# Kernel optimization log

Hardware: AMD Instinct MI355X
Metric: run time of the kernel (lower is better)

The kernel has to match this reference:

```python
import jax, jax.numpy as jnp
import numpy as np

B, S, HID = 1, 2048, 2048
H, KV, D = 16, 8, 128          # heads, kv heads, head_dim
EPS = 1e-6
THETA_T, THETA_HW = 1000000.0, 10000.0
SCALE = D ** -0.5
NEG = -1e9


def _rms(x, w):
    xf = x.astype(jnp.float32)
    var = jnp.mean(xf * xf, axis=-1, keepdims=True)
    return (w * (xf * jax.lax.rsqrt(var + EPS))).astype(x.dtype)


def _rope_cs(pos, theta, half_dim):
    # Module builds RoPE with head_dim = 2*half_dim then takes every-other freq:
    # exponents arange(0, 2*half_dim, 4) / (2*half_dim)  -> half_dim//2 freqs
    dim2 = 2 * half_dim
    inv_freq = 1.0 / theta ** (jnp.arange(0, dim2, 4, dtype=jnp.float32) / dim2)
    freqs = pos.astype(jnp.float32)[:, None] * inv_freq[None, :]   # [S, half_dim//2]
    emb = jnp.concatenate([freqs, freqs], axis=-1)                 # [S, half_dim]
    return jnp.cos(emb), jnp.sin(emb)


def _rot_half(x):
    d = x.shape[-1] // 2
    return jnp.concatenate([-x[..., d:], x[..., :d]], axis=-1)


def _apply_rope(q, k, cos, sin):
    cos = cos[None, None]  # [1,1,S,dim]
    sin = sin[None, None]
    return q * cos + _rot_half(q) * sin, k * cos + _rot_half(k) * sin


def setup_inputs() -> dict:
    key = jax.random.key(0)
    ks = jax.random.split(key, 10)
    hidden_states = jax.random.normal(ks[0], (B, S, HID), jnp.float32)
    indexes = jax.random.randint(ks[1], (3, S), 0, S)
    causal = jnp.tril(jnp.ones((S, S), bool))
    attention_mask = jnp.where(causal, 0.0, NEG).astype(jnp.float32)[None, None]
    qkv_w = jax.random.normal(ks[2], ((H + 2 * KV) * D, HID), jnp.float32) * 0.02
    qkv_b = jax.random.normal(ks[3], ((H + 2 * KV) * D,), jnp.float32) * 0.02
    o_w = jax.random.normal(ks[4], (HID, H * D), jnp.float32) * 0.02
    o_b = jax.random.normal(ks[5], (HID,), jnp.float32) * 0.02
    q_norm_w = jnp.ones((D // 2,), jnp.float32)
    k_norm_w = jnp.ones((D // 2,), jnp.float32)
    q_norm_hw_w = jnp.ones((D // 2,), jnp.float32)
    k_norm_hw_w = jnp.ones((D // 2,), jnp.float32)
    return dict(hidden_states=hidden_states, indexes=indexes, attention_mask=attention_mask,
                qkv_w=qkv_w, qkv_b=qkv_b, o_w=o_w, o_b=o_b,
                q_norm_w=q_norm_w, k_norm_w=k_norm_w,
                q_norm_hw_w=q_norm_hw_w, k_norm_hw_w=k_norm_hw_w)


def reference(hidden_states, indexes, attention_mask, qkv_w, qkv_b, o_w, o_b,
              q_norm_w, k_norm_w, q_norm_hw_w, k_norm_hw_w):
    b, s, _ = hidden_states.shape
    qkv = hidden_states @ qkv_w.T + qkv_b
    q, k, v = jnp.split(qkv, [H * D, H * D + KV * D], axis=-1)
    q = q.reshape(b, s, H, D)
    k = k.reshape(b, s, KV, D)
    v = v.reshape(b, s, KV, D)

    # split head_dim into time half and hw half
    q_t, q_hw = jnp.split(q, 2, axis=-1)
    k_t, k_hw = jnp.split(k, 2, axis=-1)
    q_t = jnp.swapaxes(_rms(q_t, q_norm_w), 1, 2)       # [B,H,S,D/2]
    k_t = jnp.swapaxes(_rms(k_t, k_norm_w), 1, 2)
    q_hw = jnp.swapaxes(_rms(q_hw, q_norm_hw_w), 1, 2)
    k_hw = jnp.swapaxes(_rms(k_hw, k_norm_hw_w), 1, 2)
    q_h, q_ww = jnp.split(q_hw, 2, axis=-1)             # [B,H,S,D/4]
    k_h, k_ww = jnp.split(k_hw, 2, axis=-1)

    cos_t, sin_t = _rope_cs(indexes[0], THETA_T, D // 2)
    q_t, k_t = _apply_rope(q_t, k_t, cos_t, sin_t)
    cos_h, sin_h = _rope_cs(indexes[1], THETA_HW, D // 4)
    q_h, k_h = _apply_rope(q_h, k_h, cos_h, sin_h)
    cos_w, sin_w = _rope_cs(indexes[2], THETA_HW, D // 4)
    q_ww, k_ww = _apply_rope(q_ww, k_ww, cos_w, sin_w)

    query = jnp.concatenate([q_t, q_h, q_ww], axis=-1)  # [B,H,S,D]
    keyst = jnp.concatenate([k_t, k_h, k_ww], axis=-1)  # [B,KV,S,D]
    value = jnp.swapaxes(v, 1, 2)                       # [B,KV,S,D]

    n_rep = H // KV
    keyst = jnp.repeat(keyst, n_rep, axis=1)
    value = jnp.repeat(value, n_rep, axis=1)

    scores = jnp.einsum('bhsd,bhtd->bhst', query, keyst) * SCALE + attention_mask
    probs = jax.nn.softmax(scores.astype(jnp.float32), axis=-1).astype(query.dtype)
    attn = jnp.einsum('bhst,bhtd->bhsd', probs, value)
    attn = jnp.swapaxes(attn, 1, 2).reshape(b, s, H * D)
    return attn @ o_w.T + o_b
```

## Files before the change

### kernel.cpp

```cpp
#include <hip/hip_runtime.h>

typedef __bf16 bf16;
typedef __bf16 bf16x4 __attribute__((ext_vector_type(4)));
typedef __bf16 bf16x8 __attribute__((ext_vector_type(8)));
typedef float f32x4 __attribute__((ext_vector_type(4)));

#define S_LEN 2048
#define HIDDEN 2048
#define NH 16
#define NKV 8
#define HD 128
#define QKV_N 4096

__device__ __forceinline__ void async_load16(const void* g, void* l) {
  __builtin_amdgcn_global_load_lds((const __attribute__((address_space(1))) unsigned int*)g,
                                   (__attribute__((address_space(3))) unsigned int*)l,
                                   16, 0, 0);
}

template <int C>
__device__ __forceinline__ float dpp_f(float x) {
  return __builtin_bit_cast(float, __builtin_amdgcn_mov_dpp(
      __builtin_bit_cast(int, x), C, 0xF, 0xF, true));
}
__device__ __forceinline__ float rowmax16(float x) {
  x = fmaxf(x, dpp_f<0x128>(x));
  x = fmaxf(x, dpp_f<0x124>(x));
  x = fmaxf(x, dpp_f<0x122>(x));
  x = fmaxf(x, dpp_f<0x121>(x));
  return x;
}
__device__ __forceinline__ float rowsum16(float x) {
  x += dpp_f<0x128>(x);
  x += dpp_f<0x124>(x);
  x += dpp_f<0x122>(x);
  x += dpp_f<0x121>(x);
  return x;
}

__global__ __launch_bounds__(256)
void cvt_f32_bf16(const float* __restrict__ src, bf16* __restrict__ dst, int n) {
  int i = (blockIdx.x * 256 + threadIdx.x) * 4;
  if (i < n) {
    float4 v = *(const float4*)(src + i);
    bf16x4 o = {(bf16)v.x, (bf16)v.y, (bf16)v.z, (bf16)v.w};
    *(bf16x4*)(dst + i) = o;
  }
}

template <int WRITE_BF16>
__global__ __launch_bounds__(256)
void gemm_bt(const bf16* __restrict__ A, const bf16* __restrict__ B,
             const float* __restrict__ bias, void* __restrict__ Cout,
             int M, int N, int K) {
  __shared__ bf16 As[128 * 32];
  __shared__ bf16 Bs[128 * 32];
  const int tid = threadIdx.x;
  const int w = tid >> 6, lane = tid & 63;
  const int quad = lane >> 4, l15 = lane & 15;
  const int wm = w >> 1, wn = w & 1;
  const int m0 = blockIdx.y * 128, n0 = blockIdx.x * 128;

  f32x4 acc[4][4];
#pragma unroll
  for (int i = 0; i < 4; i++)
#pragma unroll
    for (int j = 0; j < 4; j++) acc[i][j] = (f32x4){0.f, 0.f, 0.f, 0.f};

  const int crow = lane >> 2;
  const int ccol = (lane & 3) * 8;

  for (int k0 = 0; k0 < K; k0 += 32) {
    __syncthreads();
#pragma unroll
    for (int q = 0; q < 2; q++) {
      int c = 2 * w + q;
      async_load16(A + (size_t)(m0 + c * 16 + crow) * K + k0 + ccol, (char*)As + c * 1024);
      async_load16(B + (size_t)(n0 + c * 16 + crow) * K + k0 + ccol, (char*)Bs + c * 1024);
    }
    __syncthreads();
    bf16x8 af[4], bfr[4];
#pragma unroll
    for (int i = 0; i < 4; i++)
      af[i] = *(const bf16x8*)(As + (wm * 64 + i * 16 + l15) * 32 + quad * 8);
#pragma unroll
    for (int j = 0; j < 4; j++)
      bfr[j] = *(const bf16x8*)(Bs + (wn * 64 + j * 16 + l15) * 32 + quad * 8);
#pragma unroll
    for (int i = 0; i < 4; i++)
#pragma unroll
      for (int j = 0; j < 4; j++)
        acc[i][j] = __builtin_amdgcn_mfma_f32_16x16x32_bf16(af[i], bfr[j], acc[i][j], 0, 0, 0);
  }

#pragma unroll
  for (int i = 0; i < 4; i++) {
#pragma unroll
    for (int j = 0; j < 4; j++) {
      int col = n0 + wn * 64 + j * 16 + l15;
      float bv = bias[col];
#pragma unroll
      for (int r = 0; r < 4; r++) {
        int row = m0 + wm * 64 + i * 16 + quad * 4 + r;
        float v = acc[i][j][r] + bv;
        if (WRITE_BF16)
          ((bf16*)Cout)[(size_t)row * N + col] = (bf16)v;
        else
          ((float*)Cout)[(size_t)row * N + col] = v;
      }
    }
  }
}

__global__ __launch_bounds__(256)
void gemm_bt64(const bf16* __restrict__ A, const bf16* __restrict__ B,
               const float* __restrict__ bias, float* __restrict__ Cout,
               int M, int N, int K) {
  __shared__ bf16 As[128 * 32];
  __shared__ bf16 Bs[64 * 32];
  const int tid = threadIdx.x;
  const int w = tid >> 6, lane = tid & 63;
  const int quad = lane >> 4, l15 = lane & 15;
  const int m0 = blockIdx.y * 128, n0 = blockIdx.x * 64;

  f32x4 acc[2][4];
#pragma unroll
  for (int i = 0; i < 2; i++)
#pragma unroll
    for (int j = 0; j < 4; j++) acc[i][j] = (f32x4){0.f, 0.f, 0.f, 0.f};

  const int crow = lane >> 2;
  const int ccol = (lane & 3) * 8;

  for (int k0 = 0; k0 < K; k0 += 32) {
    __syncthreads();
#pragma unroll
    for (int q = 0; q < 2; q++) {
      int c = 2 * w + q;
      async_load16(A + (size_t)(m0 + c * 16 + crow) * K + k0 + ccol, (char*)As + c * 1024);
    }
    async_load16(B + (size_t)(n0 + w * 16 + crow) * K + k0 + ccol, (char*)Bs + w * 1024);
    __syncthreads();
    bf16x8 af[2], bfr[4];
#pragma unroll
    for (int i = 0; i < 2; i++)
      af[i] = *(const bf16x8*)(As + (w * 32 + i * 16 + l15) * 32 + quad * 8);
#pragma unroll
    for (int j = 0; j < 4; j++)
      bfr[j] = *(const bf16x8*)(Bs + (j * 16 + l15) * 32 + quad * 8);
#pragma unroll
    for (int i = 0; i < 2; i++)
#pragma unroll
      for (int j = 0; j < 4; j++)
        acc[i][j] = __builtin_amdgcn_mfma_f32_16x16x32_bf16(af[i], bfr[j], acc[i][j], 0, 0, 0);
  }

#pragma unroll
  for (int i = 0; i < 2; i++) {
#pragma unroll
    for (int j = 0; j < 4; j++) {
      int col = n0 + j * 16 + l15;
      float bv = bias[col];
#pragma unroll
      for (int r = 0; r < 4; r++) {
        int row = m0 + w * 32 + i * 16 + quad * 4 + r;
        Cout[(size_t)row * N + col] = acc[i][j][r] + bv;
      }
    }
  }
}

__global__ __launch_bounds__(128)
void normrope(const bf16* __restrict__ qkv, const int* __restrict__ idx,
              const float* __restrict__ qnw, const float* __restrict__ knw,
              const float* __restrict__ qnhw, const float* __restrict__ knhw,
              bf16* __restrict__ Qb, bf16* __restrict__ Kb) {
  const int s = blockIdx.x;
  const int y = blockIdx.y;
  const int d = threadIdx.x;

  const bool isq = (y < 16);
  const int off = isq ? (y * HD + d) : (2048 + (y - 16) * HD + d);
  float x = (float)qkv[(size_t)s * QKV_N + off];

  float ss = x * x;
#pragma unroll
  for (int o = 32; o; o >>= 1) ss += __shfl_xor(ss, o);
  float inv = rsqrtf(ss * (1.f / 64.f) + 1e-6f);
  const float* wt = (d < 64) ? (isq ? qnw : knw) : (isq ? qnhw : knhw);
  float yn = x * inv * wt[d & 63];

  float pos, invf;
  int xorm;
  bool firsthalf;
  if (d < 64) {
    pos = (float)idx[s];
    int i = d & 31;
    invf = exp2f(-(float)i * 0.6228615177913804f);
    xorm = 32;
    firsthalf = (d < 32);
  } else {
    int j = d - 64;
    int region = j >> 5;
    pos = (float)idx[(1 + region) * S_LEN + s];
    int i = j & 15;
    invf = exp2f(-(float)i * 0.8304820237218406f);
    xorm = 16;
    firsthalf = ((j & 31) < 16);
  }
  float ang = pos * invf;
  float si, co;
  sincosf(ang, &si, &co);
  float partner = __shfl_xor(yn, xorm);
  float outv = firsthalf ? (yn * co - partner * si) : (yn * co + partner * si);

  if (isq)
    Qb[((size_t)y * S_LEN + s) * HD + d] = (bf16)outv;
  else
    Kb[((size_t)(y - 16) * S_LEN + s) * HD + d] = (bf16)outv;
}

__global__ __launch_bounds__(256)
void vtrans(const bf16* __restrict__ qkv, bf16* __restrict__ VT) {
  __shared__ bf16 T[64][72];
  const int tid = threadIdx.x;
  const int s0 = blockIdx.x * 64, d0 = blockIdx.y * 64, kv = blockIdx.z;
#pragma unroll
  for (int it = 0; it < 2; it++) {
    int r = (tid >> 3) + it * 32;
    int c = (tid & 7) * 8;
    bf16x8 v = *(const bf16x8*)(qkv + (size_t)(s0 + r) * QKV_N + 3072 + kv * HD + d0 + c);
    *(bf16x8*)(&T[r][c]) = v;
  }
  __syncthreads();
#pragma unroll
  for (int it = 0; it < 2; it++) {
    int r = (tid >> 3) + it * 32;
    int c = (tid & 7) * 8;
    bf16x8 o;
#pragma unroll
    for (int j = 0; j < 8; j++) o[j] = T[c + j][r];
    *(bf16x8*)(VT + ((size_t)kv * HD + d0 + r) * S_LEN + s0 + c) = o;
  }
}

__global__ __launch_bounds__(256)
void attn_fused(const bf16* __restrict__ Qb, const bf16* __restrict__ Kb,
                const bf16* __restrict__ VT, bf16* __restrict__ attnO) {
  __shared__ bf16 Kbuf[2][8192];
  __shared__ bf16 Vbuf[8192];
  __shared__ __align__(16) bf16 Ps[4][16][72];
  const int tid = threadIdx.x;
  const int w = tid >> 6, lane = tid & 63;
  const int quad = lane >> 4, l15 = lane & 15;
  const int b = blockIdx.x;
  const int h = b & 15;
  const int g = b >> 4;
  const int qb64 = (g < 16) ? (31 - g) : (g - 16);
  const int nT = qb64 + 1;
  const int qr0 = qb64 * 64 + w * 16;
  const int kv = h >> 1;

  const bf16* Qg = Qb + (size_t)h * S_LEN * HD;
  const bf16* Kg = Kb + (size_t)kv * S_LEN * HD;
  const bf16* Vg = VT + (size_t)kv * HD * S_LEN;

  const bf16* ksrc = Kg + (size_t)(w * 16 + l15) * HD + quad * 8;
  const bf16* vsrc = Vg + (size_t)(2 * w * 16 + l15) * S_LEN + quad * 8;

  bf16x8 aq[4];
#pragma unroll
  for (int kc = 0; kc < 4; kc++)
    aq[kc] = *(const bf16x8*)(Qg + (size_t)(qr0 + l15) * HD + kc * 32 + quad * 8);

  float m2[4], li[4];
  f32x4 Oacc[8];
#pragma unroll
  for (int r = 0; r < 4; r++) { m2[r] = -1e30f; li[r] = 0.f; }
#pragma unroll
  for (int dt = 0; dt < 8; dt++) Oacc[dt] = (f32x4){0.f, 0.f, 0.f, 0.f};

  const float SC2 = 0.12751745f;

#pragma unroll
  for (int kc = 0; kc < 4; kc++)
    async_load16(ksrc + kc * 32, (char*)Kbuf[0] + (w * 4 + kc) * 1024);

  for (int tt = 0; tt < nT; ++tt) {
    const int t0 = tt << 6;
    const int cur = tt & 1;
    const bool more = (tt + 1 < nT);
    __asm__ __volatile__("s_waitcnt vmcnt(0)" ::: "memory");
    __syncthreads();

#pragma unroll
    for (int e = 0; e < 2; e++)
#pragma unroll
      for (int half = 0; half < 2; half++)
        async_load16(vsrc + (size_t)e * 16 * S_LEN + t0 + half * 32,
                     (char*)Vbuf + (half * 8 + 2 * w + e) * 1024);
    if (more) {
#pragma unroll
      for (int kc = 0; kc < 4; kc++)
        async_load16(ksrc + (size_t)(t0 + 64) * HD + kc * 32,
                     (char*)Kbuf[cur ^ 1] + (w * 4 + kc) * 1024);
    }

    f32x4 sacc[4];
#pragma unroll
    for (int nt = 0; nt < 4; nt++) {
      sacc[nt] = (f32x4){0.f, 0.f, 0.f, 0.f};
#pragma unroll
      for (int kc = 0; kc < 4; kc++) {
        bf16x8 bk = *(const bf16x8*)((const char*)Kbuf[cur] + (nt * 4 + kc) * 1024 + lane * 16);
        sacc[nt] = __builtin_amdgcn_mfma_f32_16x16x32_bf16(aq[kc], bk, sacc[nt], 0, 0, 0);
      }
    }

    const bool full = (t0 + 64 <= qr0);
#pragma unroll
    for (int r = 0; r < 4; r++) {
      const int mrow = qr0 + quad * 4 + r;
      float s0 = sacc[0][r] * SC2, s1 = sacc[1][r] * SC2;
      float s2 = sacc[2][r] * SC2, s3 = sacc[3][r] * SC2;
      if (!full) {
        int cb = t0 + l15;
        if (cb > mrow) s0 = -1e30f;
        if (cb + 16 > mrow) s1 = -1e30f;
        if (cb + 32 > mrow) s2 = -1e30f;
        if (cb + 48 > mrow) s3 = -1e30f;
      }
      float mx = rowmax16(fmaxf(fmaxf(s0, s1), fmaxf(s2, s3)));
      float mnew = fmaxf(m2[r], mx);
      float alpha = exp2f(m2[r] - mnew);
      float p0 = exp2f(s0 - mnew), p1 = exp2f(s1 - mnew);
      float p2 = exp2f(s2 - mnew), p3 = exp2f(s3 - mnew);
      float rs = rowsum16((p0 + p1) + (p2 + p3));
      li[r] = li[r] * alpha + rs;
      m2[r] = mnew;
#pragma unroll
      for (int dt = 0; dt < 8; dt++) Oacc[dt][r] *= alpha;
      Ps[w][quad * 4 + r][l15] = (bf16)p0;
      Ps[w][quad * 4 + r][16 + l15] = (bf16)p1;
      Ps[w][quad * 4 + r][32 + l15] = (bf16)p2;
      Ps[w][quad * 4 + r][48 + l15] = (bf16)p3;
    }
    __asm__ __volatile__("s_waitcnt lgkmcnt(0)" ::: "memory");
    if (more)
      __asm__ __volatile__("s_waitcnt vmcnt(4)" ::: "memory");
    else
      __asm__ __volatile__("s_waitcnt vmcnt(0)" ::: "memory");

#pragma unroll
    for (int half = 0; half < 2; half++) {
      bf16x8 ap = *(const bf16x8*)(&Ps[w][l15][half * 32 + quad * 8]);
#pragma unroll
      for (int dt = 0; dt < 8; dt++) {
        bf16x8 bv = *(const bf16x8*)((const char*)Vbuf + (half * 8 + dt) * 1024 + lane * 16);
        Oacc[dt] = __builtin_amdgcn_mfma_f32_16x16x32_bf16(ap, bv, Oacc[dt], 0, 0, 0);
      }
    }
  }

#pragma unroll
  for (int r = 0; r < 4; r++) {
    float invl = 1.f / li[r];
    int srow = qr0 + quad * 4 + r;
#pragma unroll
    for (int dt = 0; dt < 8; dt++)
      attnO[(size_t)srow * HIDDEN + h * HD + dt * 16 + l15] = (bf16)(Oacc[dt][r] * invl);
  }
}

extern "C" void kernel_launch(void* const* d_in, const int* in_sizes, int n_in,
                              void* d_out, int out_size, void* d_ws, size_t ws_size,
                              hipStream_t stream) {
  const float* hidden = (const float*)d_in[0];
  const int* idx = (const int*)d_in[1];
  const float* qkv_w = (const float*)d_in[3];
  const float* qkv_b = (const float*)d_in[4];
  const float* o_w = (const float*)d_in[5];
  const float* o_b = (const float*)d_in[6];
  const float* qnw = (const float*)d_in[7];
  const float* knw = (const float*)d_in[8];
  const float* qnhw = (const float*)d_in[9];
  const float* knhw = (const float*)d_in[10];

  char* ws = (char*)d_ws;
  bf16* hB   = (bf16*)(ws);
  bf16* qwB  = (bf16*)(ws + (8u << 20));
  bf16* qkvB = (bf16*)(ws + (24u << 20));
  bf16* Qb   = (bf16*)(ws + (40u << 20));
  bf16* Kb   = (bf16*)(ws + (48u << 20));
  bf16* VT   = (bf16*)(ws + (52u << 20));
  bf16* owB  = hB;
  bf16* attn = qwB;

  cvt_f32_bf16<<<HIDDEN * S_LEN / 1024, 256, 0, stream>>>(hidden, hB, HIDDEN * S_LEN);
  cvt_f32_bf16<<<QKV_N * HIDDEN / 1024, 256, 0, stream>>>(qkv_w, qwB, QKV_N * HIDDEN);

  gemm_bt<1><<<dim3(QKV_N / 128, S_LEN / 128), 256, 0, stream>>>(
      hB, qwB, qkv_b, qkvB, S_LEN, QKV_N, HIDDEN);

  cvt_f32_bf16<<<HIDDEN * HIDDEN / 1024, 256, 0, stream>>>(o_w, owB, HIDDEN * HIDDEN);

  normrope<<<dim3(S_LEN, 24), 128, 0, stream>>>(qkvB, idx, qnw, knw, qnhw, knhw, Qb, Kb);
  vtrans<<<dim3(S_LEN / 64, HD / 64, NKV), 256, 0, stream>>>(qkvB, VT);

  attn_fused<<<512, 256, 0, stream>>>(Qb, Kb, VT, attn);

  gemm_bt64<<<dim3(HIDDEN / 64, S_LEN / 128), 256, 0, stream>>>(
      attn, owB, o_b, (float*)d_out, S_LEN, HIDDEN, HIDDEN);
}
```

Measured before the change: 310.6 us.

## Split attention KV range across two wave groups and merge partial softmax

Doubles the attention block to 512 threads. Two groups of four waves each process half of the key tiles for the same query rows, and their partial O, max and sum values are merged through LDS at the end. V is now loaded directly into registers instead of staged in LDS. The softmax scale is folded into Q during the norm/rope step, and rescaling is skipped unless the row max grows by more than a threshold (lazy rescale). This adds parallelism per block and drops the per-element scale multiply, at the cost of losing the cross-tile K prefetch pipeline, adding extra syncs per iteration and higher register pressure.

```diff
diff --git a/kernel.cpp b/kernel.cpp
--- a/kernel.cpp
+++ b/kernel.cpp
@@ -215,7 +215,7 @@
   float outv = firsthalf ? (yn * co - partner * si) : (yn * co + partner * si);
 
   if (isq)
-    Qb[((size_t)y * S_LEN + s) * HD + d] = (bf16)outv;
+    Qb[((size_t)y * S_LEN + s) * HD + d] = (bf16)(outv * 0.12751745f);
   else
     Kb[((size_t)(y - 16) * S_LEN + s) * HD + d] = (bf16)outv;
 }
@@ -244,29 +244,31 @@
   }
 }
 
-__global__ __launch_bounds__(256)
+__global__ __launch_bounds__(512, 4)
 void attn_fused(const bf16* __restrict__ Qb, const bf16* __restrict__ Kb,
                 const bf16* __restrict__ VT, bf16* __restrict__ attnO) {
   __shared__ bf16 Kbuf[2][8192];
-  __shared__ bf16 Vbuf[8192];
-  __shared__ __align__(16) bf16 Ps[4][16][72];
+  __shared__ __align__(16) bf16 Ps[8][16][72];
   const int tid = threadIdx.x;
   const int w = tid >> 6, lane = tid & 63;
   const int quad = lane >> 4, l15 = lane & 15;
+  const int wq = w & 3, grp = w >> 2;
   const int b = blockIdx.x;
   const int h = b & 15;
   const int g = b >> 4;
   const int qb64 = (g < 16) ? (31 - g) : (g - 16);
   const int nT = qb64 + 1;
-  const int qr0 = qb64 * 64 + w * 16;
+  const int nH = nT >> 1;
+  const int L = nT - nH;
+  const int qr0 = qb64 * 64 + wq * 16;
   const int kv = h >> 1;
 
   const bf16* Qg = Qb + (size_t)h * S_LEN * HD;
   const bf16* Kg = Kb + (size_t)kv * S_LEN * HD;
   const bf16* Vg = VT + (size_t)kv * HD * S_LEN;
 
-  const bf16* ksrc = Kg + (size_t)(w * 16 + l15) * HD + quad * 8;
-  const bf16* vsrc = Vg + (size_t)(2 * w * 16 + l15) * S_LEN + quad * 8;
+  const bf16* ksrc = Kg + (size_t)(wq * 16 + l15) * HD + quad * 8;
+  const bf16* vsrc = Vg + (size_t)l15 * S_LEN + quad * 8;
 
   bf16x8 aq[4];
 #pragma unroll
@@ -280,31 +282,25 @@
 #pragma unroll
   for (int dt = 0; dt < 8; dt++) Oacc[dt] = (f32x4){0.f, 0.f, 0.f, 0.f};
 
-  const float SC2 = 0.12751745f;
-
-#pragma unroll
-  for (int kc = 0; kc < 4; kc++)
-    async_load16(ksrc + kc * 32, (char*)Kbuf[0] + (w * 4 + kc) * 1024);
-
-  for (int tt = 0; tt < nT; ++tt) {
-    const int t0 = tt << 6;
-    const int cur = tt & 1;
-    const bool more = (tt + 1 < nT);
+  for (int u = 0; u < L; ++u) {
+    const int tIdx = grp ? (nH + u) : u;
+    const bool active = grp || (u < nH);
+    const int t0 = tIdx << 6;
+
+    __syncthreads();
+    bf16x8 v0[8];
+    if (active) {
+#pragma unroll
+      for (int kc = 0; kc < 4; kc++)
+        async_load16(ksrc + (size_t)t0 * HD + kc * 32,
+                     (char*)Kbuf[grp] + (wq * 4 + kc) * 1024);
+#pragma unroll
+      for (int dt = 0; dt < 8; dt++)
+        v0[dt] = *(const bf16x8*)(vsrc + (size_t)dt * 16 * S_LEN + t0);
+    }
     __asm__ __volatile__("s_waitcnt vmcnt(0)" ::: "memory");
     __syncthreads();
-
-#pragma unroll
-    for (int e = 0; e < 2; e++)
-#pragma unroll
-      for (int half = 0; half < 2; half++)
-        async_load16(vsrc + (size_t)e * 16 * S_LEN + t0 + half * 32,
-                     (char*)Vbuf + (half * 8 + 2 * w + e) * 1024);
-    if (more) {
-#pragma unroll
-      for (int kc = 0; kc < 4; kc++)
-        async_load16(ksrc + (size_t)(t0 + 64) * HD + kc * 32,
-                     (char*)Kbuf[cur ^ 1] + (w * 4 + kc) * 1024);
-    }
+    if (!active) continue;
 
     f32x4 sacc[4];
 #pragma unroll
@@ -312,63 +308,103 @@
       sacc[nt] = (f32x4){0.f, 0.f, 0.f, 0.f};
 #pragma unroll
       for (int kc = 0; kc < 4; kc++) {
-        bf16x8 bk = *(const bf16x8*)((const char*)Kbuf[cur] + (nt * 4 + kc) * 1024 + lane * 16);
+        bf16x8 bk = *(const bf16x8*)((const char*)Kbuf[grp] + (nt * 4 + kc) * 1024 + lane * 16);
         sacc[nt] = __builtin_amdgcn_mfma_f32_16x16x32_bf16(aq[kc], bk, sacc[nt], 0, 0, 0);
       }
     }
 
     const bool full = (t0 + 64 <= qr0);
+    float mxv[4];
+    bool need = false;
 #pragma unroll
     for (int r = 0; r < 4; r++) {
-      const int mrow = qr0 + quad * 4 + r;
-      float s0 = sacc[0][r] * SC2, s1 = sacc[1][r] * SC2;
-      float s2 = sacc[2][r] * SC2, s3 = sacc[3][r] * SC2;
       if (!full) {
-        int cb = t0 + l15;
-        if (cb > mrow) s0 = -1e30f;
-        if (cb + 16 > mrow) s1 = -1e30f;
-        if (cb + 32 > mrow) s2 = -1e30f;
-        if (cb + 48 > mrow) s3 = -1e30f;
-      }
-      float mx = rowmax16(fmaxf(fmaxf(s0, s1), fmaxf(s2, s3)));
-      float mnew = fmaxf(m2[r], mx);
-      float alpha = exp2f(m2[r] - mnew);
-      float p0 = exp2f(s0 - mnew), p1 = exp2f(s1 - mnew);
-      float p2 = exp2f(s2 - mnew), p3 = exp2f(s3 - mnew);
-      float rs = rowsum16((p0 + p1) + (p2 + p3));
-      li[r] = li[r] * alpha + rs;
-      m2[r] = mnew;
-#pragma unroll
-      for (int dt = 0; dt < 8; dt++) Oacc[dt][r] *= alpha;
+        const int mrow = qr0 + quad * 4 + r;
+        const int cb = t0 + l15;
+        if (cb > mrow) sacc[0][r] = -1e30f;
+        if (cb + 16 > mrow) sacc[1][r] = -1e30f;
+        if (cb + 32 > mrow) sacc[2][r] = -1e30f;
+        if (cb + 48 > mrow) sacc[3][r] = -1e30f;
+      }
+      mxv[r] = rowmax16(fmaxf(fmaxf(sacc[0][r], sacc[1][r]), fmaxf(sacc[2][r], sacc[3][r])));
+      need = need || (mxv[r] > m2[r] + 8.f);
+    }
+    if (__any(need ? 1 : 0)) {
+#pragma unroll
+      for (int r = 0; r < 4; r++) {
+        float mnew = fmaxf(m2[r], mxv[r]);
+        float a = exp2f(m2[r] - mnew);
+        li[r] *= a;
+#pragma unroll
+        for (int dt = 0; dt < 8; dt++) Oacc[dt][r] *= a;
+        m2[r] = mnew;
+      }
+    }
+#pragma unroll
+    for (int r = 0; r < 4; r++) {
+      float p0 = exp2f(sacc[0][r] - m2[r]);
+      float p1 = exp2f(sacc[1][r] - m2[r]);
+      float p2 = exp2f(sacc[2][r] - m2[r]);
+      float p3 = exp2f(sacc[3][r] - m2[r]);
+      li[r] += rowsum16((p0 + p1) + (p2 + p3));
       Ps[w][quad * 4 + r][l15] = (bf16)p0;
       Ps[w][quad * 4 + r][16 + l15] = (bf16)p1;
       Ps[w][quad * 4 + r][32 + l15] = (bf16)p2;
       Ps[w][quad * 4 + r][48 + l15] = (bf16)p3;
     }
+
+    bf16x8 v1[8];
+#pragma unroll
+    for (int dt = 0; dt < 8; dt++)
+      v1[dt] = *(const bf16x8*)(vsrc + (size_t)dt * 16 * S_LEN + t0 + 32);
+
     __asm__ __volatile__("s_waitcnt lgkmcnt(0)" ::: "memory");
-    if (more)
-      __asm__ __volatile__("s_waitcnt vmcnt(4)" ::: "memory");
-    else
-      __asm__ __volatile__("s_waitcnt vmcnt(0)" ::: "memory");
-
-#pragma unroll
-    for (int half = 0; half < 2; half++) {
-      bf16x8 ap = *(const bf16x8*)(&Ps[w][l15][half * 32 + quad * 8]);
+
+    bf16x8 ap0 = *(const bf16x8*)(&Ps[w][l15][quad * 8]);
+#pragma unroll
+    for (int dt = 0; dt < 8; dt++)
+      Oacc[dt] = __builtin_amdgcn_mfma_f32_16x16x32_bf16(ap0, v0[dt], Oacc[dt], 0, 0, 0);
+    bf16x8 ap1 = *(const bf16x8*)(&Ps[w][l15][32 + quad * 8]);
+#pragma unroll
+    for (int dt = 0; dt < 8; dt++)
+      Oacc[dt] = __builtin_amdgcn_mfma_f32_16x16x32_bf16(ap1, v1[dt], Oacc[dt], 0, 0, 0);
+  }
+
+  __syncthreads();
+  float* Obuf = (float*)Kbuf;
+  float* MLbuf = (float*)Ps;
+  if (grp == 1) {
+#pragma unroll
+    for (int r = 0; r < 4; r++) {
+      const int row = quad * 4 + r;
+#pragma unroll
+      for (int dt = 0; dt < 8; dt++)
+        Obuf[(wq * 16 + row) * 128 + dt * 16 + l15] = Oacc[dt][r];
+      if (l15 == 0) {
+        MLbuf[(wq * 16 + row) * 2 + 0] = m2[r];
+        MLbuf[(wq * 16 + row) * 2 + 1] = li[r];
+      }
+    }
+  }
+  __syncthreads();
+  if (grp == 0) {
+#pragma unroll
+    for (int r = 0; r < 4; r++) {
+      const int row = quad * 4 + r;
+      const float mB = MLbuf[(wq * 16 + row) * 2 + 0];
+      const float lB = MLbuf[(wq * 16 + row) * 2 + 1];
+      const float m = fmaxf(m2[r], mB);
+      const float aA = exp2f(m2[r] - m);
+      const float aB = exp2f(mB - m);
+      const float invl = 1.f / (li[r] * aA + lB * aB);
+      const int srow = qr0 + row;
 #pragma unroll
       for (int dt = 0; dt < 8; dt++) {
-        bf16x8 bv = *(const bf16x8*)((const char*)Vbuf + (half * 8 + dt) * 1024 + lane * 16);
-        Oacc[dt] = __builtin_amdgcn_mfma_f32_16x16x32_bf16(ap, bv, Oacc[dt], 0, 0, 0);
-      }
-    }
-  }
-
-#pragma unroll
-  for (int r = 0; r < 4; r++) {
-    float invl = 1.f / li[r];
-    int srow = qr0 + quad * 4 + r;
-#pragma unroll
-    for (int dt = 0; dt < 8; dt++)
-      attnO[(size_t)srow * HIDDEN + h * HD + dt * 16 + l15] = (bf16)(Oacc[dt][r] * invl);
+        float ob = Obuf[(wq * 16 + row) * 128 + dt * 16 + l15];
+        attnO[(size_t)srow * HIDDEN + h * HD + dt * 16 + l15] =
+            (bf16)((Oacc[dt][r] * aA + ob * aB) * invl);
+      }
+    }
   }
 }
 
@@ -407,7 +443,7 @@
   normrope<<<dim3(S_LEN, 24), 128, 0, stream>>>(qkvB, idx, qnw, knw, qnhw, knhw, Qb, Kb);
   vtrans<<<dim3(S_LEN / 64, HD / 64, NKV), 256, 0, stream>>>(qkvB, VT);
 
-  attn_fused<<<512, 256, 0, stream>>>(Qb, Kb, VT, attn);
+  attn_fused<<<512, 512, 0, stream>>>(Qb, Kb, VT, attn);
 
   gemm_bt64<<<dim3(HIDDEN / 64, S_LEN / 128), 256, 0, stream>>>(
       attn, owB, o_b, (float*)d_out, S_LEN, HIDDEN, HIDDEN);
```

New measurement: 372.8 us. 1.2x slower.

## Split long causal attention rows across two blocks and merge partials; lazy rescale

Applied to the files above, without the earlier changes.

Query blocks with more than 16 key tiles are split into two KV-range chunks run by separate blocks, which write fp32 partial outputs plus max/sum to workspace. A new merge kernel combines the two chunks. The grid grows from 512 to 768 blocks to balance causal work. The softmax scale is folded into Q during norm/rope, and the online-softmax rescale only runs when the row max grows by more than a threshold. This adds a kernel launch and partial-output traffic.

```diff
diff --git a/kernel.cpp b/kernel.cpp
--- a/kernel.cpp
+++ b/kernel.cpp
@@ -215,7 +215,7 @@
   float outv = firsthalf ? (yn * co - partner * si) : (yn * co + partner * si);
 
   if (isq)
-    Qb[((size_t)y * S_LEN + s) * HD + d] = (bf16)outv;
+    Qb[((size_t)y * S_LEN + s) * HD + d] = (bf16)(outv * 0.12751745f);
   else
     Kb[((size_t)(y - 16) * S_LEN + s) * HD + d] = (bf16)outv;
 }
@@ -246,7 +246,8 @@
 
 __global__ __launch_bounds__(256)
 void attn_fused(const bf16* __restrict__ Qb, const bf16* __restrict__ Kb,
-                const bf16* __restrict__ VT, bf16* __restrict__ attnO) {
+                const bf16* __restrict__ VT, bf16* __restrict__ attnO,
+                float* __restrict__ Opart, float* __restrict__ Ml) {
   __shared__ bf16 Kbuf[2][8192];
   __shared__ bf16 Vbuf[8192];
   __shared__ __align__(16) bf16 Ps[4][16][72];
@@ -255,10 +256,14 @@
   const int quad = lane >> 4, l15 = lane & 15;
   const int b = blockIdx.x;
   const int h = b & 15;
-  const int g = b >> 4;
-  const int qb64 = (g < 16) ? (31 - g) : (g - 16);
-  const int nT = qb64 + 1;
-  const int qr0 = qb64 * 64 + w * 16;
+  const int cid = b >> 4;
+  int g, c;
+  if (cid < 32) { g = 16 + (cid >> 1); c = cid & 1; }
+  else          { g = cid - 32;        c = 0; }
+  const int nT = g + 1;
+  const int tBeg = c ? 16 : 0;
+  const int tEnd = c ? nT : (nT < 16 ? nT : 16);
+  const int qr0 = g * 64 + w * 16;
   const int kv = h >> 1;
 
   const bf16* Qg = Qb + (size_t)h * S_LEN * HD;
@@ -280,16 +285,15 @@
 #pragma unroll
   for (int dt = 0; dt < 8; dt++) Oacc[dt] = (f32x4){0.f, 0.f, 0.f, 0.f};
 
-  const float SC2 = 0.12751745f;
-
 #pragma unroll
   for (int kc = 0; kc < 4; kc++)
-    async_load16(ksrc + kc * 32, (char*)Kbuf[0] + (w * 4 + kc) * 1024);
-
-  for (int tt = 0; tt < nT; ++tt) {
+    async_load16(ksrc + (size_t)(tBeg << 6) * HD + kc * 32,
+                 (char*)Kbuf[tBeg & 1] + (w * 4 + kc) * 1024);
+
+  for (int tt = tBeg; tt < tEnd; ++tt) {
     const int t0 = tt << 6;
     const int cur = tt & 1;
-    const bool more = (tt + 1 < nT);
+    const bool more = (tt + 1 < tEnd);
     __asm__ __volatile__("s_waitcnt vmcnt(0)" ::: "memory");
     __syncthreads();
 
@@ -318,28 +322,39 @@
     }
 
     const bool full = (t0 + 64 <= qr0);
+    float mxv[4];
+    bool need = false;
 #pragma unroll
     for (int r = 0; r < 4; r++) {
-      const int mrow = qr0 + quad * 4 + r;
-      float s0 = sacc[0][r] * SC2, s1 = sacc[1][r] * SC2;
-      float s2 = sacc[2][r] * SC2, s3 = sacc[3][r] * SC2;
       if (!full) {
-        int cb = t0 + l15;
-        if (cb > mrow) s0 = -1e30f;
-        if (cb + 16 > mrow) s1 = -1e30f;
-        if (cb + 32 > mrow) s2 = -1e30f;
-        if (cb + 48 > mrow) s3 = -1e30f;
-      }
-      float mx = rowmax16(fmaxf(fmaxf(s0, s1), fmaxf(s2, s3)));
-      float mnew = fmaxf(m2[r], mx);
-      float alpha = exp2f(m2[r] - mnew);
-      float p0 = exp2f(s0 - mnew), p1 = exp2f(s1 - mnew);
-      float p2 = exp2f(s2 - mnew), p3 = exp2f(s3 - mnew);
-      float rs = rowsum16((p0 + p1) + (p2 + p3));
-      li[r] = li[r] * alpha + rs;
-      m2[r] = mnew;
-#pragma unroll
-      for (int dt = 0; dt < 8; dt++) Oacc[dt][r] *= alpha;
+        const int mrow = qr0 + quad * 4 + r;
+        const int cb = t0 + l15;
+        if (cb > mrow) sacc[0][r] = -1e30f;
+        if (cb + 16 > mrow) sacc[1][r] = -1e30f;
+        if (cb + 32 > mrow) sacc[2][r] = -1e30f;
+        if (cb + 48 > mrow) sacc[3][r] = -1e30f;
+      }
+      mxv[r] = rowmax16(fmaxf(fmaxf(sacc[0][r], sacc[1][r]), fmaxf(sacc[2][r], sacc[3][r])));
+      need = need || (mxv[r] > m2[r] + 8.f);
+    }
+    if (__any(need ? 1 : 0)) {
+#pragma unroll
+      for (int r = 0; r < 4; r++) {
+        float mnew = fmaxf(m2[r], mxv[r]);
+        float a = exp2f(m2[r] - mnew);
+        li[r] *= a;
+#pragma unroll
+        for (int dt = 0; dt < 8; dt++) Oacc[dt][r] *= a;
+        m2[r] = mnew;
+      }
+    }
+#pragma unroll
+    for (int r = 0; r < 4; r++) {
+      float p0 = exp2f(sacc[0][r] - m2[r]);
+      float p1 = exp2f(sacc[1][r] - m2[r]);
+      float p2 = exp2f(sacc[2][r] - m2[r]);
+      float p3 = exp2f(sacc[3][r] - m2[r]);
+      li[r] += rowsum16((p0 + p1) + (p2 + p3));
       Ps[w][quad * 4 + r][l15] = (bf16)p0;
       Ps[w][quad * 4 + r][16 + l15] = (bf16)p1;
       Ps[w][quad * 4 + r][32 + l15] = (bf16)p2;
@@ -362,13 +377,60 @@
     }
   }
 
-#pragma unroll
-  for (int r = 0; r < 4; r++) {
-    float invl = 1.f / li[r];
-    int srow = qr0 + quad * 4 + r;
-#pragma unroll
-    for (int dt = 0; dt < 8; dt++)
-      attnO[(size_t)srow * HIDDEN + h * HD + dt * 16 + l15] = (bf16)(Oacc[dt][r] * invl);
+  if (cid < 32) {
+    float* Op = Opart + (size_t)b * 64 * 128;
+    float* mlp = Ml + (size_t)b * 128;
+#pragma unroll
+    for (int r = 0; r < 4; r++) {
+      const int row = w * 16 + quad * 4 + r;
+#pragma unroll
+      for (int dt = 0; dt < 8; dt++)
+        Op[row * 128 + dt * 16 + l15] = Oacc[dt][r];
+      if (l15 == 0) {
+        mlp[row * 2 + 0] = m2[r];
+        mlp[row * 2 + 1] = li[r];
+      }
+    }
+  } else {
+#pragma unroll
+    for (int r = 0; r < 4; r++) {
+      float invl = 1.f / li[r];
+      int srow = qr0 + quad * 4 + r;
+#pragma unroll
+      for (int dt = 0; dt < 8; dt++)
+        attnO[(size_t)srow * HIDDEN + h * HD + dt * 16 + l15] = (bf16)(Oacc[dt][r] * invl);
+    }
+  }
+}
+
+__global__ __launch_bounds__(256)
+void attn_merge(const float* __restrict__ Opart, const float* __restrict__ Ml,
+                bf16* __restrict__ attnO) {
+  const int h = blockIdx.x & 15;
+  const int g = 16 + (blockIdx.x >> 4);
+  const int cid0 = (g - 16) * 2;
+  const int bA = cid0 * 16 + h, bB = (cid0 + 1) * 16 + h;
+  const float* OA = Opart + (size_t)bA * 64 * 128;
+  const float* OB = Opart + (size_t)bB * 64 * 128;
+  const float* mlA = Ml + (size_t)bA * 128;
+  const float* mlB = Ml + (size_t)bB * 128;
+  const int t = threadIdx.x;
+#pragma unroll
+  for (int it = 0; it < 8; ++it) {
+    int e = it * 256 + t;
+    int row = e >> 5, d = (e & 31) * 4;
+    float mA = mlA[row * 2], lA = mlA[row * 2 + 1];
+    float mB = mlB[row * 2], lB = mlB[row * 2 + 1];
+    float m = fmaxf(mA, mB);
+    float aA = exp2f(mA - m), aB = exp2f(mB - m);
+    float inv = 1.f / (lA * aA + lB * aB);
+    f32x4 a = *(const f32x4*)(OA + row * 128 + d);
+    f32x4 bq = *(const f32x4*)(OB + row * 128 + d);
+    int srow = g * 64 + row;
+    bf16x4 o;
+#pragma unroll
+    for (int j = 0; j < 4; j++) o[j] = (bf16)((a[j] * aA + bq[j] * aB) * inv);
+    *(bf16x4*)(attnO + (size_t)srow * HIDDEN + h * HD + d) = o;
   }
 }
 
@@ -387,14 +449,16 @@
   const float* knhw = (const float*)d_in[10];
 
   char* ws = (char*)d_ws;
-  bf16* hB   = (bf16*)(ws);
-  bf16* qwB  = (bf16*)(ws + (8u << 20));
-  bf16* qkvB = (bf16*)(ws + (24u << 20));
-  bf16* Qb   = (bf16*)(ws + (40u << 20));
-  bf16* Kb   = (bf16*)(ws + (48u << 20));
-  bf16* VT   = (bf16*)(ws + (52u << 20));
-  bf16* owB  = hB;
-  bf16* attn = qwB;
+  bf16* hB    = (bf16*)(ws);
+  bf16* qwB   = (bf16*)(ws + (8u << 20));
+  bf16* qkvB  = (bf16*)(ws + (24u << 20));
+  bf16* Qb    = (bf16*)(ws + (40u << 20));
+  bf16* Kb    = (bf16*)(ws + (48u << 20));
+  bf16* VT    = (bf16*)(ws + (52u << 20));
+  bf16* owB   = hB;
+  float* Opart = (float*)(ws + (8u << 20));
+  bf16* attn  = (bf16*)(ws + (24u << 20));
+  float* Ml   = (float*)(ws + (32u << 20));
 
   cvt_f32_bf16<<<HIDDEN * S_LEN / 1024, 256, 0, stream>>>(hidden, hB, HIDDEN * S_LEN);
   cvt_f32_bf16<<<QKV_N * HIDDEN / 1024, 256, 0, stream>>>(qkv_w, qwB, QKV_N * HIDDEN);
@@ -407,7 +471,8 @@
   normrope<<<dim3(S_LEN, 24), 128, 0, stream>>>(qkvB, idx, qnw, knw, qnhw, knhw, Qb, Kb);
   vtrans<<<dim3(S_LEN / 64, HD / 64, NKV), 256, 0, stream>>>(qkvB, VT);
 
-  attn_fused<<<512, 256, 0, stream>>>(Qb, Kb, VT, attn);
+  attn_fused<<<768, 256, 0, stream>>>(Qb, Kb, VT, attn, Opart, Ml);
+  attn_merge<<<256, 256, 0, stream>>>(Opart, Ml, attn);
 
   gemm_bt64<<<dim3(HIDDEN / 64, S_LEN / 128), 256, 0, stream>>>(
       attn, owB, o_b, (float*)d_out, S_LEN, HIDDEN, HIDDEN);
```

Result: no change. 316.8 us (+2.0%).
